# Performance work log

Measured on AMD Instinct MI355X. Metric: run time of the kernel, lower is better.

## Reference

```python
import jax, jax.numpy as jnp
import numpy as np

N, E, D, HGC, LG, NC = 20000, 320000, 256, 256, 4, 2
BN_EPS = 1e-5


def setup_inputs() -> dict:
    key = jax.random.key(0)
    ks = jax.random.split(key, 12)
    features = jax.random.normal(ks[0], (N, D), jnp.float32)
    edge_index = jax.random.randint(ks[1], (2, E), 0, N)
    edgenet_input = jax.random.uniform(ks[2], (E, 6), dtype=jnp.float32)
    edge_weight_override = jax.random.uniform(ks[3], (E,), dtype=jnp.float32)
    # ChebConv weights: K=3 weight matrices per layer; layer0 in=D==HGC so one stack works
    cheb_w = jax.random.normal(ks[4], (LG, 3, HGC, HGC), jnp.float32) * np.float32((2.0 / HGC) ** 0.5)
    w1 = jax.random.normal(ks[5], (LG * HGC, 256), jnp.float32) * np.float32((2.0 / (LG * HGC)) ** 0.5)
    b1 = jnp.zeros((256,), jnp.float32)
    bn_gamma = jnp.ones((256,), jnp.float32)
    bn_beta = jnp.zeros((256,), jnp.float32)
    bn_mean = jnp.zeros((256,), jnp.float32)
    bn_var = jnp.ones((256,), jnp.float32)
    w2 = jax.random.normal(ks[6], (256, NC), jnp.float32) * np.float32((2.0 / 256.0) ** 0.5)
    b2 = jnp.zeros((NC,), jnp.float32)
    return dict(features=features, edge_index=edge_index, edgenet_input=edgenet_input,
                edge_weight_override=edge_weight_override, cheb_w=cheb_w,
                w1=w1, b1=b1, bn_gamma=bn_gamma, bn_beta=bn_beta,
                bn_mean=bn_mean, bn_var=bn_var, w2=w2, b2=b2)


def reference(features, edge_index, edgenet_input, edge_weight_override, cheb_w,
              w1, b1, bn_gamma, bn_beta, bn_mean, bn_var, w2, b2):
    # eval mode: dropout / edge_dropout are no-ops; edge_weight_override bypasses PAE
    ew = edge_weight_override  # [E]
    row, col = edge_index[0], edge_index[1]  # source, target (PyG source_to_target)
    n = features.shape[0]
    # sym-normalized scaled Laplacian, lambda_max=2: L_hat = -D^{-1/2} A D^{-1/2} (diag 1-1=0)
    deg = jax.ops.segment_sum(ew, row, num_segments=n)
    dis = jnp.where(deg > 0, jax.lax.rsqrt(deg), 0.0)
    norm = -(dis[row] * ew * dis[col])  # [E]

    def prop(x):  # out[col] += norm * x[row]
        return jax.ops.segment_sum(norm[:, None] * x[row], col, num_segments=n)

    def cheb(x, W):  # W: [3, in, out]; Chebyshev recursion T0=x, T1=L_hat x, T2=2 L_hat T1 - T0
        tx0 = x
        tx1 = prop(x)
        out = tx0 @ W[0] + tx1 @ W[1]
        tx2 = 2.0 * prop(tx1) - tx0
        return out + tx2 @ W[2]

    h = jax.nn.relu(cheb(features, cheb_w[0]))
    jk = h
    for i in range(1, cheb_w.shape[0]):
        h = jax.nn.relu(cheb(h, cheb_w[i]))
        jk = jnp.concatenate((jk, h), axis=1)
    # classifier: Linear -> ReLU -> BatchNorm1d(eval) -> Linear
    z = jax.nn.relu(jk @ w1 + b1)
    z = (z - bn_mean) * (bn_gamma * jax.lax.rsqrt(bn_var + BN_EPS)) + bn_beta
    logit = z @ w2 + b2
    return logit, ew
```

## Files before the change

kernel.cpp:

```cpp
#include <hip/hip_runtime.h>
#include <hip/hip_bf16.h>

#define NN 20000
#define EE 320000
#define LGN 4

typedef unsigned short u16;
typedef short bf16x8 __attribute__((ext_vector_type(8)));
typedef float f32x4 __attribute__((ext_vector_type(4)));

__device__ __forceinline__ float bf2f(u16 v) {
    unsigned int u = ((unsigned int)v) << 16;
    float f; __builtin_memcpy(&f, &u, 4); return f;
}
__device__ __forceinline__ u16 f2bf(float f) {
    __hip_bfloat16 h = __float2bfloat16(f);
    u16 u; __builtin_memcpy(&u, &h, 2); return u;
}

__device__ __forceinline__ void gll16(const void* g, void* l) {
    __builtin_amdgcn_global_load_lds(
        (const __attribute__((address_space(1))) unsigned int*)g,
        (__attribute__((address_space(3))) unsigned int*)l, 16, 0, 0);
}

__global__ __launch_bounds__(256) void k_edge1(const int* __restrict__ ei,
                                               const float* __restrict__ ew,
                                               float* __restrict__ deg,
                                               int* __restrict__ counts,
                                               float* __restrict__ out_ew,
                                               int2* __restrict__ nbrs) {
    int e = blockIdx.x * 256 + threadIdx.x;
    if (blockIdx.x == 0 && threadIdx.x < 16)
        nbrs[EE + threadIdx.x] = make_int2(0, 0);
    if (e >= EE) return;
    int r = ei[e];
    float w = ew[e];
    atomicAdd(&deg[r], w);
    atomicAdd(&counts[ei[EE + e]], 1);
    out_ew[e] = w;
}

__global__ __launch_bounds__(1024) void k_scan(const int* __restrict__ counts,
                                               int* __restrict__ offs) {
    __shared__ int part[1024];
    int t = threadIdx.x;
    const int C = (NN + 1023) / 1024;
    int lo = t * C, hi = min(lo + C, NN);
    int s = 0;
    for (int i = lo; i < hi; i++) s += counts[i];
    part[t] = s;
    __syncthreads();
    for (int off = 1; off < 1024; off <<= 1) {
        int add = (t >= off) ? part[t - off] : 0;
        __syncthreads();
        part[t] += add;
        __syncthreads();
    }
    int base = part[t] - s;
    for (int i = lo; i < hi; i++) { offs[i] = base; base += counts[i]; }
    if (t == 1023) offs[NN] = part[1023];
}

__global__ __launch_bounds__(256) void k_scatter(const int* __restrict__ ei,
                                                 const float* __restrict__ ew,
                                                 const float* __restrict__ deg,
                                                 const int* __restrict__ offs,
                                                 int* __restrict__ cursor,
                                                 int2* __restrict__ nbrs) {
    int e = blockIdx.x * 256 + threadIdx.x;
    if (e >= EE) return;
    int r = ei[e], c = ei[EE + e];
    float dr = deg[r], dc = deg[c];
    float ir = (dr > 0.f) ? rsqrtf(dr) : 0.f;
    float ic = (dc > 0.f) ? rsqrtf(dc) : 0.f;
    float nm = -(ir * ew[e] * ic);
    int pidx = offs[c] + atomicAdd(&cursor[c], 1);
    nbrs[pidx] = make_int2(r, __float_as_int(nm));
}

__device__ __forceinline__ void castB_chunk(const float* __restrict__ src,
                                            u16* __restrict__ dst, int u) {
    int l = u & 63, f = (u >> 6) & 15, s = u >> 10;
    int col = f * 16 + (l & 15);
    int kb = s * 32 + ((l >> 4) << 3);
    u16 tmp[8];
#pragma unroll
    for (int j = 0; j < 8; j++) tmp[j] = f2bf(src[(size_t)(kb + j) * 256 + col]);
    *(uint4*)(dst + (size_t)u * 8) = *(uint4*)tmp;
}

__global__ __launch_bounds__(256) void k_prep(
    const float* __restrict__ features, u16* __restrict__ xb,
    const float* __restrict__ cheb_w, u16* __restrict__ chebT,
    const float* __restrict__ w1, u16* __restrict__ w1T,
    const float* __restrict__ g, const float* __restrict__ be,
    const float* __restrict__ mn, const float* __restrict__ vr,
    float* __restrict__ sc, float* __restrict__ sh) {
    int tid = blockIdx.x * 256 + threadIdx.x;
    if (tid < NN * 256) {
        xb[tid] = f2bf(features[tid]);
        return;
    }
    tid -= NN * 256;
    if (tid < 4 * 24576) {
        int set = tid / 24576, u = tid - set * 24576;
        castB_chunk(cheb_w + (size_t)set * 768 * 256, chebT + (size_t)set * 768 * 256, u);
        return;
    }
    tid -= 4 * 24576;
    if (tid < 32768) {
        castB_chunk(w1, w1T, tid);
        return;
    }
    tid -= 32768;
    if (tid < 256) {
        float s = g[tid] * rsqrtf(vr[tid] + 1e-5f);
        sc[tid] = s;
        sh[tid] = be[tid] - mn[tid] * s;
    }
}

__global__ __launch_bounds__(256) void k_prop(const u16* __restrict__ x, int ldx,
                                              const u16* __restrict__ xsub, int ldsub,
                                              int dotx2,
                                              u16* __restrict__ out, int ldo,
                                              const int* __restrict__ offs,
                                              const int2* __restrict__ nbrs) {
    int c = __builtin_amdgcn_readfirstlane(blockIdx.x * 4 + (threadIdx.x >> 6));
    int lane = threadIdx.x & 63;
    int s = offs[c], e = offs[c + 1];
    float a0 = 0.f, a1 = 0.f, a2 = 0.f, a3 = 0.f;
    for (int i = s; i < e; i += 16) {
        int2 mm[16];
        ushort4 xv[16];
        bool g1 = (i + 4 < e), g2 = (i + 8 < e), g3 = (i + 12 < e);
#pragma unroll
        for (int j = 0; j < 4; j++) mm[j] = nbrs[i + j];
        if (g1) {
#pragma unroll
            for (int j = 4; j < 8; j++) mm[j] = nbrs[i + j];
        }
        if (g2) {
#pragma unroll
            for (int j = 8; j < 12; j++) mm[j] = nbrs[i + j];
        }
        if (g3) {
#pragma unroll
            for (int j = 12; j < 16; j++) mm[j] = nbrs[i + j];
        }
#pragma unroll
        for (int j = 0; j < 4; j++)
            xv[j] = *(const ushort4*)(x + (size_t)mm[j].x * ldx + lane * 4);
        if (g1) {
#pragma unroll
            for (int j = 4; j < 8; j++)
                xv[j] = *(const ushort4*)(x + (size_t)mm[j].x * ldx + lane * 4);
        }
        if (g2) {
#pragma unroll
            for (int j = 8; j < 12; j++)
                xv[j] = *(const ushort4*)(x + (size_t)mm[j].x * ldx + lane * 4);
        }
        if (g3) {
#pragma unroll
            for (int j = 12; j < 16; j++)
                xv[j] = *(const ushort4*)(x + (size_t)mm[j].x * ldx + lane * 4);
        }
#pragma unroll
        for (int j = 0; j < 4; j++) {
            float w = (i + j < e) ? __int_as_float(mm[j].y) : 0.f;
            a0 += w * bf2f(xv[j].x);
            a1 += w * bf2f(xv[j].y);
            a2 += w * bf2f(xv[j].z);
            a3 += w * bf2f(xv[j].w);
        }
        if (g1) {
#pragma unroll
            for (int j = 4; j < 8; j++) {
                float w = (i + j < e) ? __int_as_float(mm[j].y) : 0.f;
                a0 += w * bf2f(xv[j].x);
                a1 += w * bf2f(xv[j].y);
                a2 += w * bf2f(xv[j].z);
                a3 += w * bf2f(xv[j].w);
            }
        }
        if (g2) {
#pragma unroll
            for (int j = 8; j < 12; j++) {
                float w = (i + j < e) ? __int_as_float(mm[j].y) : 0.f;
                a0 += w * bf2f(xv[j].x);
                a1 += w * bf2f(xv[j].y);
                a2 += w * bf2f(xv[j].z);
                a3 += w * bf2f(xv[j].w);
            }
        }
        if (g3) {
#pragma unroll
            for (int j = 12; j < 16; j++) {
                float w = (i + j < e) ? __int_as_float(mm[j].y) : 0.f;
                a0 += w * bf2f(xv[j].x);
                a1 += w * bf2f(xv[j].y);
                a2 += w * bf2f(xv[j].z);
                a3 += w * bf2f(xv[j].w);
            }
        }
    }
    if (dotx2) {
        ushort4 xs = *(const ushort4*)(xsub + (size_t)c * ldsub + lane * 4);
        a0 = 2.f * a0 - bf2f(xs.x);
        a1 = 2.f * a1 - bf2f(xs.y);
        a2 = 2.f * a2 - bf2f(xs.z);
        a3 = 2.f * a3 - bf2f(xs.w);
    }
    ushort4 o;
    o.x = f2bf(a0); o.y = f2bf(a1); o.z = f2bf(a2); o.w = f2bf(a3);
    *(ushort4*)(out + (size_t)c * ldo + lane * 4) = o;
}

__global__ __launch_bounds__(128, 2) void k_gemm(
    const u16* __restrict__ A0, const u16* __restrict__ A1,
    const u16* __restrict__ A2,
    int lda0, int lda1, int lda2,
    int K, const u16* __restrict__ Bf, const u16* __restrict__ Bf2,
    const u16* __restrict__ jkb,
    int mode,
    u16* __restrict__ outb, int ldob,
    const float* __restrict__ bias, const float* __restrict__ sc,
    const float* __restrict__ sh,
    const float* __restrict__ w2, const float* __restrict__ b2,
    float* __restrict__ outlog) {
    __shared__ __align__(16) u16 lds[12544];
    int t = threadIdx.x;
    int wv = t >> 6, l = t & 63;
    int q = l >> 4, l16 = l & 15;
    int m0 = blockIdx.x * 32;
    int n0 = wv * 128;
    const int steps = K >> 5;

    f32x4 acc[2][8] = {};

    int arow = m0 + wv * 16 + l16;

    auto stageA = [&](int buf, int s) {
        int kt = s * 32;
        int ch = kt >> 8;
        const u16* ap;
        int la;
        if (ch == 0) { ap = A0; la = lda0; }
        else if (ch == 1) { ap = A1; la = lda1; }
        else { ap = A2; la = lda2; }
        gll16(ap + (size_t)arow * la + (kt & 255) + q * 8, lds + buf * 1024 + wv * 512);
    };

    const u16* bfw = Bf + (size_t)(wv * 8) * 512 + l * 8;
    auto loadB = [&](bf16x8* dst, int s) {
#pragma unroll
        for (int j = 0; j < 8; j++)
            dst[j] = *(const bf16x8*)(bfw + (size_t)s * 8192 + j * 512);
    };
    auto comp = [&](int buf, const bf16x8* b) {
        const u16* base = lds + buf * 1024;
        bf16x8 a[2];
#pragma unroll
        for (int mh = 0; mh < 2; mh++)
            a[mh] = *(const bf16x8*)(base + mh * 512 + l * 8);
#pragma unroll
        for (int mh = 0; mh < 2; mh++)
#pragma unroll
            for (int j = 0; j < 8; j++)
                acc[mh][j] =
                    __builtin_amdgcn_mfma_f32_16x16x32_bf16(a[mh], b[j], acc[mh][j], 0, 0, 0);
    };

    bf16x8 bA[8], bB[8];
    loadB(bA, 0);
    stageA(0, 0);
    stageA(1, 1);
    stageA(2, 2);
    for (int s = 0; s < steps; s += 2) {
        if (s == 0)               asm volatile("s_waitcnt vmcnt(2)" ::: "memory");
        else                      asm volatile("s_waitcnt vmcnt(10)" ::: "memory");
        __builtin_amdgcn_s_barrier();
        __builtin_amdgcn_sched_barrier(0);
        loadB(bB, s + 1);
        __builtin_amdgcn_sched_barrier(0);
        if (s + 3 < steps) stageA((s + 3) & 3, s + 3);
        __builtin_amdgcn_sched_barrier(0);
        comp(s & 3, bA);
        asm volatile("s_waitcnt vmcnt(10)" ::: "memory");
        __builtin_amdgcn_s_barrier();
        __builtin_amdgcn_sched_barrier(0);
        if (s + 2 < steps) loadB(bA, s + 2);
        __builtin_amdgcn_sched_barrier(0);
        if (s + 4 < steps) stageA((s + 4) & 3, s + 4);
        __builtin_amdgcn_sched_barrier(0);
        comp((s + 1) & 3, bB);
    }
    __syncthreads();

    if (mode == 0) {
        u16* Cs = lds + 4096 + wv * 4352;
#pragma unroll
        for (int mh = 0; mh < 2; mh++)
#pragma unroll
            for (int j = 0; j < 8; j++)
#pragma unroll
                for (int i = 0; i < 4; i++) {
                    float v = acc[mh][j][i];
                    v = v > 0.f ? v : 0.f;
                    Cs[(mh * 16 + q * 4 + i) * 136 + j * 16 + l16] = f2bf(v);
                }
#pragma unroll
        for (int jj = 0; jj < 8; jj++) {
            int f = jj * 64 + l;
            int r = f >> 4, cc = (f & 15) * 8;
            uint4 cv = *(const uint4*)&Cs[r * 136 + cc];
            int row = m0 + r;
            if (row < NN) *(uint4*)(outb + (size_t)row * ldob + n0 + cc) = cv;
        }
        return;
    }

    u16* Csh = lds + 4096;
#pragma unroll
    for (int mh = 0; mh < 2; mh++)
#pragma unroll
        for (int j = 0; j < 8; j++)
#pragma unroll
            for (int i = 0; i < 4; i++) {
                float v = acc[mh][j][i];
                v = v > 0.f ? v : 0.f;
                Csh[(mh * 16 + q * 4 + i) * 264 + n0 + j * 16 + l16] = f2bf(v);
            }
    __syncthreads();

#pragma unroll
    for (int mh = 0; mh < 2; mh++)
#pragma unroll
        for (int j = 0; j < 8; j++)
            acc[mh][j] = (f32x4){0.f, 0.f, 0.f, 0.f};

    const u16* bfw2 = Bf2 + (size_t)(wv * 8) * 512 + l * 8;
    auto loadB2 = [&](bf16x8* dst, int s) {
#pragma unroll
        for (int j = 0; j < 8; j++)
            dst[j] = *(const bf16x8*)(bfw2 + (size_t)s * 8192 + j * 512);
    };
    auto stageB = [&](int buf, int s) {
        int kt = s * 32;
        const u16* ap = jkb + (size_t)(kt >> 8) * 256;
        gll16(ap + (size_t)arow * 1024 + (kt & 255) + q * 8, lds + buf * 1024 + wv * 512);
    };
    auto comph = [&](int ss, const bf16x8* b) {
        bf16x8 a[2];
#pragma unroll
        for (int mh = 0; mh < 2; mh++)
            a[mh] = *(const bf16x8*)(Csh + (mh * 16 + l16) * 264 + ss * 32 + q * 8);
#pragma unroll
        for (int mh = 0; mh < 2; mh++)
#pragma unroll
            for (int j = 0; j < 8; j++)
                acc[mh][j] =
                    __builtin_amdgcn_mfma_f32_16x16x32_bf16(a[mh], b[j], acc[mh][j], 0, 0, 0);
    };

    loadB2(bA, 0);
    stageB(0, 0);
    stageB(1, 1);
    stageB(2, 2);
    for (int s = 0; s < 24; s += 2) {
        if (s == 0)               asm volatile("s_waitcnt vmcnt(2)" ::: "memory");
        else                      asm volatile("s_waitcnt vmcnt(10)" ::: "memory");
        __builtin_amdgcn_s_barrier();
        __builtin_amdgcn_sched_barrier(0);
        loadB2(bB, s + 1);
        __builtin_amdgcn_sched_barrier(0);
        if (s + 3 < 24) stageB((s + 3) & 3, s + 3);
        __builtin_amdgcn_sched_barrier(0);
        comp(s & 3, bA);
        asm volatile("s_waitcnt vmcnt(10)" ::: "memory");
        __builtin_amdgcn_s_barrier();
        __builtin_amdgcn_sched_barrier(0);
        loadB2(bA, s + 2);
        __builtin_amdgcn_sched_barrier(0);
        if (s + 4 < 24) stageB((s + 4) & 3, s + 4);
        __builtin_amdgcn_sched_barrier(0);
        comp((s + 1) & 3, bB);
    }
    for (int s = 24; s < 32; s += 2) {
        loadB2(bB, s + 1);
        comph(s - 24, bA);
        if (s + 2 < 32) loadB2(bA, s + 2);
        comph(s - 23, bB);
    }

    {
        float bi[8], s4[8], h4[8], wa[8], wb[8];
#pragma unroll
        for (int j = 0; j < 8; j++) {
            int col = n0 + j * 16 + l16;
            bi[j] = bias[col];
            s4[j] = sc[col];
            h4[j] = sh[col];
            wa[j] = w2[2 * col];
            wb[j] = w2[2 * col + 1];
        }
        float* red = (float*)lds;
#pragma unroll
        for (int mh = 0; mh < 2; mh++)
#pragma unroll
            for (int i = 0; i < 4; i++) {
                float p0 = 0.f, p1 = 0.f;
#pragma unroll
                for (int j = 0; j < 8; j++) {
                    float v = acc[mh][j][i] + bi[j];
                    v = v > 0.f ? v : 0.f;
                    v = v * s4[j] + h4[j];
                    p0 += v * wa[j];
                    p1 += v * wb[j];
                }
#pragma unroll
                for (int off = 1; off < 16; off <<= 1) {
                    p0 += __shfl_xor(p0, off, 64);
                    p1 += __shfl_xor(p1, off, 64);
                }
                if (l16 == 0) {
                    int rl = mh * 16 + q * 4 + i;
                    red[(wv * 32 + rl) * 2 + 0] = p0;
                    red[(wv * 32 + rl) * 2 + 1] = p1;
                }
            }
        __syncthreads();
        if (t < 64) {
            int rl = t >> 1, cp = t & 1;
            float v = red[(0 * 32 + rl) * 2 + cp] + red[(1 * 32 + rl) * 2 + cp];
            int row = m0 + rl;
            if (row < NN) outlog[(size_t)row * 2 + cp] = v + b2[cp];
        }
    }
}

extern "C" void kernel_launch(void* const* d_in, const int* in_sizes, int n_in,
                              void* d_out, int out_size, void* d_ws, size_t ws_size,
                              hipStream_t stream) {
    const float* features = (const float*)d_in[0];
    const int* ei = (const int*)d_in[1];
    const float* ew = (const float*)d_in[3];
    const float* cheb_w = (const float*)d_in[4];
    const float* w1 = (const float*)d_in[5];
    const float* b1 = (const float*)d_in[6];
    const float* g = (const float*)d_in[7];
    const float* be = (const float*)d_in[8];
    const float* mn = (const float*)d_in[9];
    const float* vr = (const float*)d_in[10];
    const float* w2 = (const float*)d_in[11];
    const float* b2 = (const float*)d_in[12];
    float* out = (float*)d_out;

    char* p = (char*)d_ws;
    auto alloc = [&](size_t bytes) -> char* {
        char* r = p;
        p += (bytes + 255) & ~(size_t)255;
        return r;
    };
    float* deg = (float*)alloc((size_t)NN * 4);
    int* counts = (int*)alloc((size_t)(NN + 1) * 4);
    int* cursor = (int*)alloc((size_t)NN * 4);
    size_t zero_bytes = (size_t)(p - (char*)deg);
    int* offs = (int*)alloc((size_t)(NN + 1) * 4);
    int2* nbrs = (int2*)alloc((size_t)(EE + 16) * 8);
    u16* xb = (u16*)alloc((size_t)NN * 256 * 2);
    u16* tx1 = (u16*)alloc((size_t)NN * 256 * 2);
    u16* tx2 = (u16*)alloc((size_t)NN * 256 * 2);
    u16* jk = (u16*)alloc((size_t)NN * 1024 * 2);
    u16* chebT = (u16*)alloc((size_t)LGN * 3 * 256 * 256 * 2);
    u16* w1T = (u16*)alloc((size_t)1024 * 256 * 2);
    float* sc = (float*)alloc(256 * 4);
    float* sh = (float*)alloc(256 * 4);

    hipMemsetAsync(deg, 0, zero_bytes, stream);
    k_edge1<<<(EE + 255) / 256, 256, 0, stream>>>(ei, ew, deg, counts, out + (size_t)NN * 2,
                                                  nbrs);
    k_scan<<<1, 1024, 0, stream>>>(counts, offs);
    k_scatter<<<(EE + 255) / 256, 256, 0, stream>>>(ei, ew, deg, offs, cursor, nbrs);
    const int prep_items = NN * 256 + 4 * 24576 + 32768 + 256;
    k_prep<<<(prep_items + 255) / 256, 256, 0, stream>>>(features, xb, cheb_w, chebT, w1, w1T,
                                                         g, be, mn, vr, sc, sh);

    const int gg = (NN + 31) / 32;
    for (int i = 0; i < LGN; i++) {
        const u16* x = (i == 0) ? xb : (jk + (size_t)(i - 1) * 256);
        int ldx = (i == 0) ? 256 : 1024;
        k_prop<<<NN / 4, 256, 0, stream>>>(x, ldx, (const u16*)nullptr, 0, 0, tx1, 256, offs,
                                           nbrs);
        k_prop<<<NN / 4, 256, 0, stream>>>(tx1, 256, x, ldx, 1, tx2, 256, offs, nbrs);
        if (i < LGN - 1) {
            k_gemm<<<gg, 128, 0, stream>>>(
                x, tx1, tx2, ldx, 256, 256, 768, chebT + (size_t)i * 256 * 768,
                (const u16*)nullptr, (const u16*)nullptr, 0, jk + (size_t)i * 256, 1024,
                (const float*)nullptr, (const float*)nullptr, (const float*)nullptr,
                (const float*)nullptr, (const float*)nullptr, (float*)nullptr);
        } else {
            k_gemm<<<gg, 128, 0, stream>>>(
                x, tx1, tx2, ldx, 256, 256, 768, chebT + (size_t)i * 256 * 768,
                w1T, jk, 2, (u16*)nullptr, 0, b1, sc, sh, w2, b2, out);
        }
    }
}
```

Measured before the change: 439.3 us.

## Fuse second Chebyshev propagation into GEMM and fold T2 algebra into weights

Folds the Chebyshev T2 = 2·L·T1 − T0 recursion into the weights (W0−W2, W1, 2·W2), so the second propagation no longer subtracts x. That propagation is then computed inside the GEMM kernel: each block gathers L·T1 for its 32 rows into LDS and uses it as the last K-chunk. This drops one prop kernel launch per layer and the tx2 write and read round-trip through global memory. In exchange the GEMM blocks first run a serial gather over 16 rows per wave before the MFMA pipeline, which may hurt latency hiding, uses more LDS and so risks occupancy, and computing W0−W2 in bf16 changes rounding.

```diff
diff --git a/kernel.cpp b/kernel.cpp
--- a/kernel.cpp
+++ b/kernel.cpp
@@ -90,6 +90,24 @@
     *(uint4*)(dst + (size_t)u * 8) = *(uint4*)tmp;
 }
 
+__device__ __forceinline__ void castB_chunk_cheb(const float* __restrict__ src,
+                                                 u16* __restrict__ dst, int u) {
+    int l = u & 63, f = (u >> 6) & 15, s = u >> 10;
+    int col = f * 16 + (l & 15);
+    int kb = s * 32 + ((l >> 4) << 3);
+    u16 tmp[8];
+#pragma unroll
+    for (int j = 0; j < 8; j++) {
+        int k = kb + j;
+        float v;
+        if (k < 256)       v = src[(size_t)k * 256 + col] - src[(size_t)(k + 512) * 256 + col];
+        else if (k < 512)  v = src[(size_t)k * 256 + col];
+        else               v = 2.f * src[(size_t)k * 256 + col];
+        tmp[j] = f2bf(v);
+    }
+    *(uint4*)(dst + (size_t)u * 8) = *(uint4*)tmp;
+}
+
 __global__ __launch_bounds__(256) void k_prep(
     const float* __restrict__ features, u16* __restrict__ xb,
     const float* __restrict__ cheb_w, u16* __restrict__ chebT,
@@ -105,7 +123,7 @@
     tid -= NN * 256;
     if (tid < 4 * 24576) {
         int set = tid / 24576, u = tid - set * 24576;
-        castB_chunk(cheb_w + (size_t)set * 768 * 256, chebT + (size_t)set * 768 * 256, u);
+        castB_chunk_cheb(cheb_w + (size_t)set * 768 * 256, chebT + (size_t)set * 768 * 256, u);
         return;
     }
     tid -= 4 * 24576;
@@ -122,9 +140,7 @@
 }
 
 __global__ __launch_bounds__(256) void k_prop(const u16* __restrict__ x, int ldx,
-                                              const u16* __restrict__ xsub, int ldsub,
-                                              int dotx2,
-                                              u16* __restrict__ out, int ldo,
+                                              u16* __restrict__ out,
                                               const int* __restrict__ offs,
                                               const int2* __restrict__ nbrs) {
     int c = __builtin_amdgcn_readfirstlane(blockIdx.x * 4 + (threadIdx.x >> 6));
@@ -206,51 +222,125 @@
             }
         }
     }
-    if (dotx2) {
-        ushort4 xs = *(const ushort4*)(xsub + (size_t)c * ldsub + lane * 4);
-        a0 = 2.f * a0 - bf2f(xs.x);
-        a1 = 2.f * a1 - bf2f(xs.y);
-        a2 = 2.f * a2 - bf2f(xs.z);
-        a3 = 2.f * a3 - bf2f(xs.w);
-    }
     ushort4 o;
     o.x = f2bf(a0); o.y = f2bf(a1); o.z = f2bf(a2); o.w = f2bf(a3);
-    *(ushort4*)(out + (size_t)c * ldo + lane * 4) = o;
+    *(ushort4*)(out + (size_t)c * 256 + lane * 4) = o;
 }
 
 __global__ __launch_bounds__(128, 2) void k_gemm(
-    const u16* __restrict__ A0, const u16* __restrict__ A1,
-    const u16* __restrict__ A2,
-    int lda0, int lda1, int lda2,
-    int K, const u16* __restrict__ Bf, const u16* __restrict__ Bf2,
+    const u16* __restrict__ A0, int lda0,
+    const u16* __restrict__ TX,
+    const int* __restrict__ offs, const int2* __restrict__ nbrs,
+    const u16* __restrict__ Bf, const u16* __restrict__ Bf2,
     const u16* __restrict__ jkb,
-    int mode,
-    u16* __restrict__ outb, int ldob,
+    int mode, u16* __restrict__ outb,
     const float* __restrict__ bias, const float* __restrict__ sc,
-    const float* __restrict__ sh,
-    const float* __restrict__ w2, const float* __restrict__ b2,
-    float* __restrict__ outlog) {
-    __shared__ __align__(16) u16 lds[12544];
+    const float* __restrict__ sh, const float* __restrict__ w2,
+    const float* __restrict__ b2, float* __restrict__ outlog) {
+    __shared__ __align__(16) u16 lds[20992];
     int t = threadIdx.x;
     int wv = t >> 6, l = t & 63;
     int q = l >> 4, l16 = l & 15;
     int m0 = blockIdx.x * 32;
     int n0 = wv * 128;
-    const int steps = K >> 5;
+    u16* Y = lds + 4096;
+    u16* H3 = lds + 12544;
+
+    for (int r = 0; r < 16; r++) {
+        int c = m0 + wv * 16 + r;
+        int s0 = offs[c], e0 = offs[c + 1];
+        float a0 = 0.f, a1 = 0.f, a2 = 0.f, a3 = 0.f;
+        for (int i = s0; i < e0; i += 16) {
+            int2 mm[16];
+            ushort4 xv[16];
+            bool g1 = (i + 4 < e0), g2 = (i + 8 < e0), g3 = (i + 12 < e0);
+#pragma unroll
+            for (int j = 0; j < 4; j++) mm[j] = nbrs[i + j];
+            if (g1) {
+#pragma unroll
+                for (int j = 4; j < 8; j++) mm[j] = nbrs[i + j];
+            }
+            if (g2) {
+#pragma unroll
+                for (int j = 8; j < 12; j++) mm[j] = nbrs[i + j];
+            }
+            if (g3) {
+#pragma unroll
+                for (int j = 12; j < 16; j++) mm[j] = nbrs[i + j];
+            }
+#pragma unroll
+            for (int j = 0; j < 4; j++)
+                xv[j] = *(const ushort4*)(TX + (size_t)mm[j].x * 256 + l * 4);
+            if (g1) {
+#pragma unroll
+                for (int j = 4; j < 8; j++)
+                    xv[j] = *(const ushort4*)(TX + (size_t)mm[j].x * 256 + l * 4);
+            }
+            if (g2) {
+#pragma unroll
+                for (int j = 8; j < 12; j++)
+                    xv[j] = *(const ushort4*)(TX + (size_t)mm[j].x * 256 + l * 4);
+            }
+            if (g3) {
+#pragma unroll
+                for (int j = 12; j < 16; j++)
+                    xv[j] = *(const ushort4*)(TX + (size_t)mm[j].x * 256 + l * 4);
+            }
+#pragma unroll
+            for (int j = 0; j < 4; j++) {
+                float w = (i + j < e0) ? __int_as_float(mm[j].y) : 0.f;
+                a0 += w * bf2f(xv[j].x);
+                a1 += w * bf2f(xv[j].y);
+                a2 += w * bf2f(xv[j].z);
+                a3 += w * bf2f(xv[j].w);
+            }
+            if (g1) {
+#pragma unroll
+                for (int j = 4; j < 8; j++) {
+                    float w = (i + j < e0) ? __int_as_float(mm[j].y) : 0.f;
+                    a0 += w * bf2f(xv[j].x);
+                    a1 += w * bf2f(xv[j].y);
+                    a2 += w * bf2f(xv[j].z);
+                    a3 += w * bf2f(xv[j].w);
+                }
+            }
+            if (g2) {
+#pragma unroll
+                for (int j = 8; j < 12; j++) {
+                    float w = (i + j < e0) ? __int_as_float(mm[j].y) : 0.f;
+                    a0 += w * bf2f(xv[j].x);
+                    a1 += w * bf2f(xv[j].y);
+                    a2 += w * bf2f(xv[j].z);
+                    a3 += w * bf2f(xv[j].w);
+                }
+            }
+            if (g3) {
+#pragma unroll
+                for (int j = 12; j < 16; j++) {
+                    float w = (i + j < e0) ? __int_as_float(mm[j].y) : 0.f;
+                    a0 += w * bf2f(xv[j].x);
+                    a1 += w * bf2f(xv[j].y);
+                    a2 += w * bf2f(xv[j].z);
+                    a3 += w * bf2f(xv[j].w);
+                }
+            }
+        }
+        ushort4 o;
+        o.x = f2bf(a0); o.y = f2bf(a1); o.z = f2bf(a2); o.w = f2bf(a3);
+        *(ushort4*)(Y + (wv * 16 + r) * 264 + l * 4) = o;
+    }
+    __syncthreads();
 
     f32x4 acc[2][8] = {};
-
     int arow = m0 + wv * 16 + l16;
 
     auto stageA = [&](int buf, int s) {
         int kt = s * 32;
-        int ch = kt >> 8;
         const u16* ap;
         int la;
-        if (ch == 0) { ap = A0; la = lda0; }
-        else if (ch == 1) { ap = A1; la = lda1; }
-        else { ap = A2; la = lda2; }
-        gll16(ap + (size_t)arow * la + (kt & 255) + q * 8, lds + buf * 1024 + wv * 512);
+        if (kt < 256) { ap = A0; la = lda0; }
+        else          { ap = TX; la = 256; kt -= 256; }
+        gll16(ap + (size_t)arow * la + kt + q * 8, lds + buf * 1024 + wv * 512);
     };
 
     const u16* bfw = Bf + (size_t)(wv * 8) * 512 + l * 8;
@@ -265,6 +355,18 @@
 #pragma unroll
         for (int mh = 0; mh < 2; mh++)
             a[mh] = *(const bf16x8*)(base + mh * 512 + l * 8);
+#pragma unroll
+        for (int mh = 0; mh < 2; mh++)
+#pragma unroll
+            for (int j = 0; j < 8; j++)
+                acc[mh][j] =
+                    __builtin_amdgcn_mfma_f32_16x16x32_bf16(a[mh], b[j], acc[mh][j], 0, 0, 0);
+    };
+    auto comp_y = [&](int ss, const bf16x8* b) {
+        bf16x8 a[2];
+#pragma unroll
+        for (int mh = 0; mh < 2; mh++)
+            a[mh] = *(const bf16x8*)(Y + (mh * 16 + l16) * 264 + ss * 32 + q * 8);
 #pragma unroll
         for (int mh = 0; mh < 2; mh++)
 #pragma unroll
@@ -278,24 +380,30 @@
     stageA(0, 0);
     stageA(1, 1);
     stageA(2, 2);
-    for (int s = 0; s < steps; s += 2) {
-        if (s == 0)               asm volatile("s_waitcnt vmcnt(2)" ::: "memory");
-        else                      asm volatile("s_waitcnt vmcnt(10)" ::: "memory");
+    for (int s = 0; s < 16; s += 2) {
+        if (s == 0) asm volatile("s_waitcnt vmcnt(2)" ::: "memory");
+        else        asm volatile("s_waitcnt vmcnt(10)" ::: "memory");
         __builtin_amdgcn_s_barrier();
         __builtin_amdgcn_sched_barrier(0);
         loadB(bB, s + 1);
         __builtin_amdgcn_sched_barrier(0);
-        if (s + 3 < steps) stageA((s + 3) & 3, s + 3);
+        if (s + 3 < 16) stageA((s + 3) & 3, s + 3);
         __builtin_amdgcn_sched_barrier(0);
         comp(s & 3, bA);
         asm volatile("s_waitcnt vmcnt(10)" ::: "memory");
         __builtin_amdgcn_s_barrier();
         __builtin_amdgcn_sched_barrier(0);
-        if (s + 2 < steps) loadB(bA, s + 2);
-        __builtin_amdgcn_sched_barrier(0);
-        if (s + 4 < steps) stageA((s + 4) & 3, s + 4);
+        loadB(bA, s + 2);
+        __builtin_amdgcn_sched_barrier(0);
+        if (s + 4 < 16) stageA((s + 4) & 3, s + 4);
         __builtin_amdgcn_sched_barrier(0);
         comp((s + 1) & 3, bB);
+    }
+    for (int s = 16; s < 24; s += 2) {
+        loadB(bB, s + 1);
+        comp_y(s - 16, bA);
+        if (s + 2 < 24) loadB(bA, s + 2);
+        comp_y(s - 15, bB);
     }
     __syncthreads();
 
@@ -317,12 +425,11 @@
             int r = f >> 4, cc = (f & 15) * 8;
             uint4 cv = *(const uint4*)&Cs[r * 136 + cc];
             int row = m0 + r;
-            if (row < NN) *(uint4*)(outb + (size_t)row * ldob + n0 + cc) = cv;
+            if (row < NN) *(uint4*)(outb + (size_t)row * 1024 + n0 + cc) = cv;
         }
         return;
     }
 
-    u16* Csh = lds + 4096;
 #pragma unroll
     for (int mh = 0; mh < 2; mh++)
 #pragma unroll
@@ -331,7 +438,7 @@
             for (int i = 0; i < 4; i++) {
                 float v = acc[mh][j][i];
                 v = v > 0.f ? v : 0.f;
-                Csh[(mh * 16 + q * 4 + i) * 264 + n0 + j * 16 + l16] = f2bf(v);
+                H3[(mh * 16 + q * 4 + i) * 264 + n0 + j * 16 + l16] = f2bf(v);
             }
     __syncthreads();
 
@@ -356,7 +463,7 @@
         bf16x8 a[2];
 #pragma unroll
         for (int mh = 0; mh < 2; mh++)
-            a[mh] = *(const bf16x8*)(Csh + (mh * 16 + l16) * 264 + ss * 32 + q * 8);
+            a[mh] = *(const bf16x8*)(H3 + (mh * 16 + l16) * 264 + ss * 32 + q * 8);
 #pragma unroll
         for (int mh = 0; mh < 2; mh++)
 #pragma unroll
@@ -370,8 +477,8 @@
     stageB(1, 1);
     stageB(2, 2);
     for (int s = 0; s < 24; s += 2) {
-        if (s == 0)               asm volatile("s_waitcnt vmcnt(2)" ::: "memory");
-        else                      asm volatile("s_waitcnt vmcnt(10)" ::: "memory");
+        if (s == 0) asm volatile("s_waitcnt vmcnt(2)" ::: "memory");
+        else        asm volatile("s_waitcnt vmcnt(10)" ::: "memory");
         __builtin_amdgcn_s_barrier();
         __builtin_amdgcn_sched_barrier(0);
         loadB2(bB, s + 1);
@@ -472,7 +579,6 @@
     int2* nbrs = (int2*)alloc((size_t)(EE + 16) * 8);
     u16* xb = (u16*)alloc((size_t)NN * 256 * 2);
     u16* tx1 = (u16*)alloc((size_t)NN * 256 * 2);
-    u16* tx2 = (u16*)alloc((size_t)NN * 256 * 2);
     u16* jk = (u16*)alloc((size_t)NN * 1024 * 2);
     u16* chebT = (u16*)alloc((size_t)LGN * 3 * 256 * 256 * 2);
     u16* w1T = (u16*)alloc((size_t)1024 * 256 * 2);
@@ -492,19 +598,17 @@
     for (int i = 0; i < LGN; i++) {
         const u16* x = (i == 0) ? xb : (jk + (size_t)(i - 1) * 256);
         int ldx = (i == 0) ? 256 : 1024;
-        k_prop<<<NN / 4, 256, 0, stream>>>(x, ldx, (const u16*)nullptr, 0, 0, tx1, 256, offs,
-                                           nbrs);
-        k_prop<<<NN / 4, 256, 0, stream>>>(tx1, 256, x, ldx, 1, tx2, 256, offs, nbrs);
+        k_prop<<<NN / 4, 256, 0, stream>>>(x, ldx, tx1, offs, nbrs);
         if (i < LGN - 1) {
             k_gemm<<<gg, 128, 0, stream>>>(
-                x, tx1, tx2, ldx, 256, 256, 768, chebT + (size_t)i * 256 * 768,
-                (const u16*)nullptr, (const u16*)nullptr, 0, jk + (size_t)i * 256, 1024,
+                x, ldx, tx1, offs, nbrs, chebT + (size_t)i * 256 * 768,
+                (const u16*)nullptr, (const u16*)nullptr, 0, jk + (size_t)i * 256,
                 (const float*)nullptr, (const float*)nullptr, (const float*)nullptr,
                 (const float*)nullptr, (const float*)nullptr, (float*)nullptr);
         } else {
             k_gemm<<<gg, 128, 0, stream>>>(
-                x, tx1, tx2, ldx, 256, 256, 768, chebT + (size_t)i * 256 * 768,
-                w1T, jk, 2, (u16*)nullptr, 0, b1, sc, sh, w2, b2, out);
-        }
-    }
-}
+                x, ldx, tx1, offs, nbrs, chebT + (size_t)i * 256 * 768,
+                w1T, jk, 2, (u16*)nullptr, b1, sc, sh, w2, b2, out);
+        }
+    }
+}
```

Result: slower. 488.4 us (+11.2%).
